# Performance work log

Measured on AMD Instinct MI355X. Metric: run time of the kernel, lower is better.

Reference implementation:

```python
import jax, jax.numpy as jnp
import numpy as np

B, S, P = 16, 1024, 1024
D, H, HD = 128, 8, 16      # embed_dim, num_heads, head_dim (qkv_dim)
MS = 32                    # ms_hidden_dim
E = 524288                 # number of edges
TANH_CLIP = 10.0
TEMP = 1.0
EPS = 1e-9


def setup_inputs() -> dict:
    key = jax.random.key(0)
    ks = jax.random.split(key, 12)
    inv = lambda n: 1.0 / np.sqrt(n)
    return {
        "x1": jax.random.normal(ks[0], (B, S, D), jnp.float32),
        "x2": jax.random.normal(ks[1], (B, P, D), jnp.float32),
        "b_idx": jax.random.randint(ks[2], (E,), 0, B, jnp.int32),
        "s_idx": jax.random.randint(ks[3], (E,), 0, S, jnp.int32),
        "p_idx": jax.random.randint(ks[4], (E,), 0, P, jnp.int32),
        "w": jax.random.uniform(ks[5], (E,), jnp.float32),
        "Wqv1": jax.random.normal(ks[6], (D, 2 * D), jnp.float32) * inv(D),
        "Wkv2": jax.random.normal(ks[7], (D, 2 * D), jnp.float32) * inv(D),
        "Wo1": jax.random.normal(ks[8], (D, D), jnp.float32) * inv(D),
        "Wo2": jax.random.normal(ks[9], (D, D), jnp.float32) * inv(D),
        "msW1": jax.random.normal(ks[10], (H, 2, MS), jnp.float32) * inv(2),
        "msb1": jnp.zeros((H, MS), jnp.float32),
        "msW2": jax.random.normal(ks[11], (H, MS, 1), jnp.float32) * inv(MS),
        "msb2": jnp.zeros((H, 1), jnp.float32),
    }


def _mixed_scores(logits, w, msW1, msb1, msW2, msb2):
    # logits: [E, H], w: [E] -> per-head 2->MS->1 MLP (MatNet MixedScoreFF)
    mixed = jnp.stack([logits, jnp.broadcast_to(w[:, None], logits.shape)], axis=-1)  # [E,H,2]
    hid = jax.nn.relu(jnp.einsum('ehi,him->ehm', mixed, msW1) + msb1)  # [E,H,MS]
    out = (jnp.einsum('ehm,hmo->eho', hid, msW2) + msb2)[..., 0]       # [E,H]
    return TANH_CLIP * jnp.tanh(out) / TEMP


def _group_softmax_combine(logits, values, gid, num_groups):
    # logits: [E,H], values: [E,H,HD]; exp -> segment-sum denom -> weighted scatter
    el = jnp.exp(logits)
    denom = jax.ops.segment_sum(el, gid, num_segments=num_groups)      # [G,H]
    attn = el / (denom[gid] + EPS)                                      # [E,H]
    return jax.ops.segment_sum(attn[:, :, None] * values, gid, num_segments=num_groups)  # [G,H,HD]


def reference(x1, x2, b_idx, s_idx, p_idx, w, Wqv1, Wkv2, Wo1, Wo2, msW1, msb1, msW2, msb2):
    qv1 = (x1 @ Wqv1).reshape(B, S, 2, H, HD)   # [B,S,2,H,HD]
    kv2 = (x2 @ Wkv2).reshape(B, P, 2, H, HD)
    row_flat = b_idx * S + s_idx                # [E]
    col_flat = b_idx * P + p_idx
    qv1_e = qv1.reshape(B * S, 2, H, HD)[row_flat]   # [E,2,H,HD]
    kv2_e = kv2.reshape(B * P, 2, H, HD)[col_flat]
    q, v1 = qv1_e[:, 0], qv1_e[:, 1]
    k, v2 = kv2_e[:, 0], kv2_e[:, 1]
    logits = jnp.einsum('ehd,ehd->eh', q, k) / np.sqrt(HD).astype(np.float32)
    logits = _mixed_scores(logits, w, msW1, msb1, msW2, msb2)
    row_heads = _group_softmax_combine(logits, v2, row_flat, B * S)  # [B*S,H,HD]
    col_heads = _group_softmax_combine(logits, v1, col_flat, B * P)  # [B*P,H,HD]
    h1 = row_heads.reshape(B, S, H * HD) @ Wo1
    h2 = col_heads.reshape(B, P, H * HD) @ Wo2
    return h1, h2
```

## Files before the change

kernel.cpp:

```cpp
#include <hip/hip_runtime.h>
#include <hip/hip_fp16.h>
#include <math.h>

#define BB   16
#define SS   1024
#define PP   1024
#define HH   8
#define MSS  32
#define EE   524288
#define NROW (BB*SS)
#define NCOL (BB*PP)
#define ESTRIDE 5
#define NRWB 512
#define NB   128
#define CHUNK 4096
#define GCAP 96

#define GLL(gp, lp) __builtin_amdgcn_global_load_lds( \
    (const __attribute__((address_space(1))) void*)(gp), \
    (__attribute__((address_space(3))) void*)(lp), 16, 0, 0)

__global__ __launch_bounds__(256, 2) void proj_kernel(
        const float* __restrict__ x1, const float* __restrict__ x2,
        const float* __restrict__ Wqv1, const float* __restrict__ Wkv2,
        float* __restrict__ qf, float* __restrict__ kf,
        __half* __restrict__ v1h, __half* __restrict__ v2h) {
    __shared__ float As[64 * 132];
    __shared__ float Bs[2][16 * 256];
    int t = threadIdx.x;
    int bid = blockIdx.x;
    int matrix = bid >> 8;
    int mb = bid & 255;
    const float* A  = matrix ? x2 : x1;
    const float* Bm = matrix ? Wkv2 : Wqv1;
    const float* Arow = A + (size_t)mb * 64 * 128;

    int tx = t & 31, ty = t >> 5;
#pragma unroll
    for (int li = 0; li < 8; li++) {
        int idx = li * 256 + t;
        int r = idx >> 5, p = idx & 31;
        *(float4*)&As[r * 132 + 4 * p] = *(const float4*)(Arow + r * 128 + 4 * p);
    }
#pragma unroll
    for (int li = 0; li < 4; li++) {
        int idx = li * 256 + t;
        GLL(Bm + 4 * idx, &Bs[0][4 * idx]);
    }

    float4 accL[8], accR[8];
#pragma unroll
    for (int i = 0; i < 8; i++) {
        accL[i] = make_float4(0.f, 0.f, 0.f, 0.f);
        accR[i] = make_float4(0.f, 0.f, 0.f, 0.f);
    }

    __syncthreads();

    for (int kc = 0; kc < 8; kc++) {
        if (kc < 7) {
            const float* src = Bm + (size_t)(kc + 1) * 16 * 256;
            float* dst = Bs[(kc + 1) & 1];
#pragma unroll
            for (int li = 0; li < 4; li++) {
                int idx = li * 256 + t;
                GLL(src + 4 * idx, dst + 4 * idx);
            }
        }
        const float* Bcur = Bs[kc & 1];
#pragma unroll
        for (int kq = 0; kq < 4; kq++) {
            float4 a4[8];
#pragma unroll
            for (int i = 0; i < 8; i++)
                a4[i] = *(const float4*)&As[(ty + 8 * i) * 132 + kc * 16 + kq * 4];
#pragma unroll
            for (int kk = 0; kk < 4; kk++) {
                float4 bL = *(const float4*)&Bcur[(kq * 4 + kk) * 256 + 4 * tx];
                float4 bR = *(const float4*)&Bcur[(kq * 4 + kk) * 256 + 128 + 4 * tx];
#pragma unroll
                for (int i = 0; i < 8; i++) {
                    float av = ((const float*)&a4[i])[kk];
                    accL[i].x = fmaf(av, bL.x, accL[i].x);
                    accL[i].y = fmaf(av, bL.y, accL[i].y);
                    accL[i].z = fmaf(av, bL.z, accL[i].z);
                    accL[i].w = fmaf(av, bL.w, accL[i].w);
                    accR[i].x = fmaf(av, bR.x, accR[i].x);
                    accR[i].y = fmaf(av, bR.y, accR[i].y);
                    accR[i].z = fmaf(av, bR.z, accR[i].z);
                    accR[i].w = fmaf(av, bR.w, accR[i].w);
                }
            }
        }
        __syncthreads();
    }

    float* Cq = matrix ? kf : qf;
    __half* Cv = matrix ? v2h : v1h;
#pragma unroll
    for (int i = 0; i < 8; i++) {
        int row = mb * 64 + ty + 8 * i;
        *(float4*)(Cq + (size_t)row * 128 + 4 * tx) = accL[i];
        __half2* p = (__half2*)(Cv + (size_t)row * 128 + 4 * tx);
        p[0] = __halves2half2(__float2half(accR[i].x), __float2half(accR[i].y));
        p[1] = __halves2half2(__float2half(accR[i].z), __float2half(accR[i].w));
    }
}

__global__ __launch_bounds__(256) void outp_kernel(
        const float* __restrict__ rh, const float* __restrict__ ch,
        const float* __restrict__ Wo1, const float* __restrict__ Wo2,
        float* __restrict__ out) {
    __shared__ float As[64 * 132];
    __shared__ float Bs[2][16 * 128];
    int t = threadIdx.x;
    int matrix = blockIdx.x >> 8;
    int mb = blockIdx.x & 255;
    const float* A  = matrix ? ch : rh;
    const float* Bm = matrix ? Wo2 : Wo1;
    float* C = out + (size_t)matrix * NROW * 128;
    const float* Arow = A + (size_t)mb * 64 * 128;

    int tx = t & 31, ty = t >> 5;
#pragma unroll
    for (int li = 0; li < 8; li++) {
        int idx = li * 256 + t;
        int r = idx >> 5, p = idx & 31;
        *(float4*)&As[r * 132 + 4 * p] = *(const float4*)(Arow + r * 128 + 4 * p);
    }
#pragma unroll
    for (int li = 0; li < 2; li++) {
        int idx = li * 256 + t;
        GLL(Bm + 4 * idx, &Bs[0][4 * idx]);
    }

    float4 acc4[8];
#pragma unroll
    for (int i = 0; i < 8; i++) acc4[i] = make_float4(0.f, 0.f, 0.f, 0.f);

    __syncthreads();

    for (int kc = 0; kc < 8; kc++) {
        if (kc < 7) {
            const float* src = Bm + (size_t)(kc + 1) * 16 * 128;
            float* dst = Bs[(kc + 1) & 1];
#pragma unroll
            for (int li = 0; li < 2; li++) {
                int idx = li * 256 + t;
                GLL(src + 4 * idx, dst + 4 * idx);
            }
        }
        const float* Bcur = Bs[kc & 1];
#pragma unroll
        for (int kq = 0; kq < 4; kq++) {
            float4 a4[8];
#pragma unroll
            for (int i = 0; i < 8; i++)
                a4[i] = *(const float4*)&As[(ty + 8 * i) * 132 + kc * 16 + kq * 4];
#pragma unroll
            for (int kk = 0; kk < 4; kk++) {
                float4 b4 = *(const float4*)&Bcur[(kq * 4 + kk) * 128 + 4 * tx];
#pragma unroll
                for (int i = 0; i < 8; i++) {
                    float av = ((const float*)&a4[i])[kk];
                    acc4[i].x = fmaf(av, b4.x, acc4[i].x);
                    acc4[i].y = fmaf(av, b4.y, acc4[i].y);
                    acc4[i].z = fmaf(av, b4.z, acc4[i].z);
                    acc4[i].w = fmaf(av, b4.w, acc4[i].w);
                }
            }
        }
        __syncthreads();
    }

#pragma unroll
    for (int i = 0; i < 8; i++) {
        int row = mb * 64 + ty + 8 * i;
        *(float4*)(C + (size_t)row * 128 + 4 * tx) = acc4[i];
    }
}

__global__ __launch_bounds__(1024) void hist_kernel(
        const int* __restrict__ b_idx, const int* __restrict__ s_idx,
        const int* __restrict__ p_idx, unsigned int* __restrict__ ph) {
    __shared__ unsigned int lh[16384];
    int t = threadIdx.x;
#pragma unroll
    for (int i = 0; i < 16; i++) lh[t + 1024 * i] = 0;
    __syncthreads();
    int base = blockIdx.x * CHUNK;
#pragma unroll
    for (int k = 0; k < 4; k++) {
        int e = base + k * 1024 + t;
        int b = b_idx[e];
        int rbin = (b << 10) + s_idx[e];
        int cbin = 16384 + (b << 10) + p_idx[e];
        atomicAdd(&lh[rbin >> 1], 1u << (16 * (rbin & 1)));
        atomicAdd(&lh[cbin >> 1], 1u << (16 * (cbin & 1)));
    }
    __syncthreads();
    unsigned int* dst = ph + (size_t)blockIdx.x * 16384;
#pragma unroll
    for (int i = 0; i < 16; i++) dst[t + 1024 * i] = lh[t + 1024 * i];
}

__global__ __launch_bounds__(128) void scan1_kernel(
        const unsigned int* __restrict__ ph, int* __restrict__ pbase,
        int* __restrict__ tot) {
    int bin = blockIdx.x * 128 + threadIdx.x;
    int word = bin >> 1;
    int sh = 16 * (bin & 1);
    int run = 0;
#pragma unroll 8
    for (int j = 0; j < NB; j++) {
        unsigned int v = ph[(size_t)j * 16384 + word];
        pbase[(size_t)j * 32768 + bin] = run;
        run += (v >> sh) & 0xffff;
    }
    tot[bin] = run;
}

__global__ __launch_bounds__(1024) void scan2_kernel(
        const int* __restrict__ tot, int* __restrict__ offs) {
    __shared__ int sdata[1024];
    int side = blockIdx.x;
    int t = threadIdx.x;
    const int* c = tot + side * 16384;
    int* o = offs + side * (16384 + 1);
    int base = t * 16;
    int loc[16];
    int run = 0;
#pragma unroll
    for (int i = 0; i < 16; i++) { loc[i] = run; run += c[base + i]; }
    sdata[t] = run;
    __syncthreads();
    for (int st = 1; st < 1024; st <<= 1) {
        int v = (t >= st) ? sdata[t - st] : 0;
        __syncthreads();
        sdata[t] += v;
        __syncthreads();
    }
    int excl = sdata[t] - run;
#pragma unroll
    for (int i = 0; i < 16; i++) o[base + i] = excl + loc[i];
    if (t == 1023) o[16384] = sdata[1023];
}

__global__ __launch_bounds__(1024) void pos_kernel(
        const int* __restrict__ b_idx, const int* __restrict__ s_idx,
        const int* __restrict__ p_idx, const float* __restrict__ w,
        const int* __restrict__ pbase, const int* __restrict__ offs,
        int4* __restrict__ ebuf) {
    __shared__ int cur[16384];
    int t = threadIdx.x;
    {
        const int* src = pbase + (size_t)blockIdx.x * 32768 + 16384;
        const int* oc = offs + (16384 + 1);
#pragma unroll
        for (int i = 0; i < 16; i++) {
            int idx = t + 1024 * i;
            cur[idx] = oc[idx] + src[idx];
        }
    }
    __syncthreads();
    int base = blockIdx.x * CHUNK;
    int rowr[4], colr[4], pcr[4];
    float wr[4];
#pragma unroll
    for (int k = 0; k < 4; k++) {
        int e = base + k * 1024 + t;
        int b = b_idx[e];
        rowr[k] = (b << 10) + s_idx[e];
        colr[k] = (b << 10) + p_idx[e];
        wr[k] = w[e];
        pcr[k] = atomicAdd(&cur[colr[k]], 1);
    }
    __syncthreads();
    {
        const int* src = pbase + (size_t)blockIdx.x * 32768;
#pragma unroll
        for (int i = 0; i < 16; i++) {
            int idx = t + 1024 * i;
            cur[idx] = offs[idx] + src[idx];
        }
    }
    __syncthreads();
#pragma unroll
    for (int k = 0; k < 4; k++) {
        int pr = atomicAdd(&cur[rowr[k]], 1);
        ebuf[pr] = make_int4(rowr[k], colr[k], __float_as_int(wr[k]), pcr[k]);
    }
}

__global__ __launch_bounds__(256) void edge_kernel(
        const float* __restrict__ qf, const float* __restrict__ kf,
        const int4* __restrict__ ebuf, const int* __restrict__ offs_row,
        const float* __restrict__ msW1, const float* __restrict__ msb1,
        const float* __restrict__ msW2, const float* __restrict__ msb2,
        float* __restrict__ entr, float* __restrict__ entc) {
    __shared__ float4 sPk[8 * 33];
    __shared__ float sB2[8];
    int t = threadIdx.x;
    {
        int h = t >> 5, m = t & 31;
        sPk[h * 33 + m] = make_float4(msW1[h * 64 + m], msW1[h * 64 + 32 + m],
                                      msb1[h * 32 + m], msW2[h * 32 + m]);
    }
    if (t < 8) sB2[t] = msb2[t];
    __syncthreads();

    int x = blockIdx.x & 7;
    int ridx = blockIdx.x >> 3;
    int wv = t >> 6;
    int lane = t & 63;
    int l = lane & 7;
    int g = lane >> 3;

    int rl = ridx * 4 + wv;
    int row = ((x + ((rl >> 10) << 3)) << 10) + (rl & 1023);
    int s = offs_row[row];
    int cnt = offs_row[row + 1] - s;

    int hh = 2 * (l & 3) + (l >> 2);
    const float4* wp = &sPk[hh * 33];
    float bias2 = sB2[hh];

    const float4* qp4 = (const float4*)(qf + (size_t)row * 128);
    float4 q0 = qp4[l], q1 = qp4[8 + l], q2 = qp4[16 + l], q3 = qp4[24 + l];

    for (int j0 = 0; j0 < cnt; j0 += 8) {
        int j = j0 + g;
        if (j < cnt) {
            int pos = s + j;
            int4 rec = ebuf[pos];
            int col = rec.y;
            float we = __int_as_float(rec.z);
            int pc = rec.w;

            const float4* kp4 = (const float4*)(kf + (size_t)col * 128);
            float p0, p1, p2, p3;
            {
                float4 k4 = kp4[l];
                p0 = fmaf(q0.x, k4.x, fmaf(q0.y, k4.y, fmaf(q0.z, k4.z, q0.w * k4.w)));
            }
            {
                float4 k4 = kp4[8 + l];
                p1 = fmaf(q1.x, k4.x, fmaf(q1.y, k4.y, fmaf(q1.z, k4.z, q1.w * k4.w)));
            }
            {
                float4 k4 = kp4[16 + l];
                p2 = fmaf(q2.x, k4.x, fmaf(q2.y, k4.y, fmaf(q2.z, k4.z, q2.w * k4.w)));
            }
            {
                float4 k4 = kp4[24 + l];
                p3 = fmaf(q3.x, k4.x, fmaf(q3.y, k4.y, fmaf(q3.z, k4.z, q3.w * k4.w)));
            }
            p0 += __shfl_xor(p0, 1); p0 += __shfl_xor(p0, 2);
            p1 += __shfl_xor(p1, 1); p1 += __shfl_xor(p1, 2);
            p2 += __shfl_xor(p2, 1); p2 += __shfl_xor(p2, 2);
            p3 += __shfl_xor(p3, 1); p3 += __shfl_xor(p3, 2);

            int js = l & 3;
            float dot = js == 0 ? p0 : (js == 1 ? p1 : (js == 2 ? p2 : p3));
            float logit = dot * 0.25f;

            float outv = bias2;
#pragma unroll 4
            for (int m = 0; m < MSS; m++) {
                float4 c = wp[m];
                float hid = fmaf(logit, c.x, fmaf(we, c.y, c.z));
                hid = fmaxf(hid, 0.f);
                outv = fmaf(hid, c.w, outv);
            }
            float u  = __expf(outv + outv);
            float th = 1.0f - 2.0f * __builtin_amdgcn_rcpf(u + 1.0f);
            float ev = __expf(10.0f * th);
            __half evh = __float2half(ev);

            float* er = entr + (size_t)pos * ESTRIDE;
            float* ec = entc + (size_t)pc * ESTRIDE;
            ((__half*)er)[2 + hh] = evh;
            ((__half*)ec)[2 + hh] = evh;
            if (l == 0) {
                er[0] = __int_as_float(col);
                ec[0] = __int_as_float(row);
            }
        }
    }
}

__global__ __launch_bounds__(128) void combine_kernel(
        const float* __restrict__ entr, const float* __restrict__ entc,
        const int* __restrict__ offs_row, const int* __restrict__ offs_col,
        const __half* __restrict__ v1h, const __half* __restrict__ v2h,
        float* __restrict__ row_heads, float* __restrict__ col_heads) {
    __shared__ float sE[GCAP * ESTRIDE];
    int x = blockIdx.x & 7;
    int r = blockIdx.x >> 3;
    int which = r >> 10;
    int sidx = r & 1023;
    int b = x + ((which & 1) << 3);
    int gl = (b << 10) + sidx;

    int t = threadIdx.x;
    int h = t >> 4;
    const float* ent; const __half* vals; const int* offs; float* outp;
    if (which < 2) { ent = entr; vals = v2h; offs = offs_row; outp = row_heads; }
    else           { ent = entc; vals = v1h; offs = offs_col; outp = col_heads; }
    int s = offs[gl], e_ = offs[gl + 1];
    int cnt = e_ - s;
    int cap = cnt < GCAP ? cnt : GCAP;

    const float* gsrc = ent + (size_t)s * ESTRIDE;
    for (int i = t; i < cap * ESTRIDE; i += 128) sE[i] = gsrc[i];
    __syncthreads();

    float acc = 0.f, den = 0.f;
#pragma unroll 8
    for (int i = 0; i < cap; i++) {
        const float* en = &sE[i * ESTRIDE];
        int other = __float_as_int(en[0]);
        float ev = __half2float(((const __half*)en)[2 + h]);
        float v = __half2float(vals[(size_t)other * 128 + t]);
        acc = fmaf(ev, v, acc);
        den += ev;
    }
    for (int i = cap; i < cnt; i++) {
        const float* en = gsrc + (size_t)i * ESTRIDE;
        int other = __float_as_int(en[0]);
        float ev = __half2float(((const __half*)en)[2 + h]);
        float v = __half2float(vals[(size_t)other * 128 + t]);
        acc = fmaf(ev, v, acc);
        den += ev;
    }
    outp[(size_t)gl * 128 + t] = acc / (den + 1e-9f);
}

extern "C" void kernel_launch(void* const* d_in, const int* in_sizes, int n_in,
                              void* d_out, int out_size, void* d_ws, size_t ws_size,
                              hipStream_t stream) {
    const float* x1   = (const float*)d_in[0];
    const float* x2   = (const float*)d_in[1];
    const int* b_idx  = (const int*)d_in[2];
    const int* s_idx  = (const int*)d_in[3];
    const int* p_idx  = (const int*)d_in[4];
    const float* w    = (const float*)d_in[5];
    const float* Wqv1 = (const float*)d_in[6];
    const float* Wkv2 = (const float*)d_in[7];
    const float* Wo1  = (const float*)d_in[8];
    const float* Wo2  = (const float*)d_in[9];
    const float* msW1 = (const float*)d_in[10];
    const float* msb1 = (const float*)d_in[11];
    const float* msW2 = (const float*)d_in[12];
    const float* msb2 = (const float*)d_in[13];
    float* out = (float*)d_out;

    float* qf = (float*)d_ws;
    float* kf = qf + (size_t)NROW * 128;
    __half* v1h = (__half*)(kf + (size_t)NCOL * 128);
    __half* v2h = v1h + (size_t)NROW * 128;
    float* entr = (float*)(v2h + (size_t)NCOL * 128);
    float* entc = entr + (size_t)EE * ESTRIDE;
    float* row_heads = entc + (size_t)EE * ESTRIDE;
    float* col_heads = row_heads + (size_t)NROW * 128;
    int4* ebuf = (int4*)(col_heads + (size_t)NCOL * 128);
    int* offs = (int*)(ebuf + EE);
    int* tot  = offs + 2 * (16384 + 1);
    unsigned int* ph = (unsigned int*)entc;
    int* pbase = (int*)row_heads;

    hist_kernel<<<NB, 1024, 0, stream>>>(b_idx, s_idx, p_idx, ph);
    scan1_kernel<<<256, 128, 0, stream>>>(ph, pbase, tot);
    scan2_kernel<<<2, 1024, 0, stream>>>(tot, offs);
    pos_kernel<<<NB, 1024, 0, stream>>>(b_idx, s_idx, p_idx, w, pbase, offs, ebuf);

    proj_kernel<<<512, 256, 0, stream>>>(x1, x2, Wqv1, Wkv2, qf, kf, v1h, v2h);

    edge_kernel<<<8 * NRWB, 256, 0, stream>>>(
        qf, kf, ebuf, offs, msW1, msb1, msW2, msb2, entr, entc);

    combine_kernel<<<2 * NROW, 128, 0, stream>>>(
        entr, entc, offs, offs + (16384 + 1), v1h, v2h, row_heads, col_heads);

    outp_kernel<<<512, 256, 0, stream>>>(row_heads, col_heads, Wo1, Wo2, out);
}
```

Before: 241.9 us.

## Split mixed-score MLP hidden units across lane groups with shuffle exchange

The 32-unit hidden layer of the per-head mixed-score MLP was computed serially by each lane, each step reading packed weights from shared memory. Now each of the 8 lane groups holds 4 hidden units' weights in registers. Logits and edge weights are exchanged among groups via shuffles, and partial sums are shuffled back and reduced. This cuts per-lane arithmetic and LDS reads from 32 to 4 units per edge, at the cost of about 24 shuffles. The loop becomes branch-free with clamped indices so all lanes take part in the shuffles.

Measured after the change: 242.3 us. About the same (+0.2%).

```diff
diff --git a/kernel.cpp b/kernel.cpp
--- a/kernel.cpp
+++ b/kernel.cpp
@@ -322,61 +322,84 @@
     int cnt = offs_row[row + 1] - s;
 
     int hh = 2 * (l & 3) + (l >> 2);
-    const float4* wp = &sPk[hh * 33];
     float bias2 = sB2[hh];
+    float4 c0 = sPk[hh * 33 + 4 * g + 0];
+    float4 c1 = sPk[hh * 33 + 4 * g + 1];
+    float4 c2 = sPk[hh * 33 + 4 * g + 2];
+    float4 c3 = sPk[hh * 33 + 4 * g + 3];
 
     const float4* qp4 = (const float4*)(qf + (size_t)row * 128);
     float4 q0 = qp4[l], q1 = qp4[8 + l], q2 = qp4[16 + l], q3 = qp4[24 + l];
 
     for (int j0 = 0; j0 < cnt; j0 += 8) {
         int j = j0 + g;
-        if (j < cnt) {
-            int pos = s + j;
-            int4 rec = ebuf[pos];
-            int col = rec.y;
-            float we = __int_as_float(rec.z);
-            int pc = rec.w;
-
-            const float4* kp4 = (const float4*)(kf + (size_t)col * 128);
-            float p0, p1, p2, p3;
-            {
-                float4 k4 = kp4[l];
-                p0 = fmaf(q0.x, k4.x, fmaf(q0.y, k4.y, fmaf(q0.z, k4.z, q0.w * k4.w)));
-            }
-            {
-                float4 k4 = kp4[8 + l];
-                p1 = fmaf(q1.x, k4.x, fmaf(q1.y, k4.y, fmaf(q1.z, k4.z, q1.w * k4.w)));
-            }
-            {
-                float4 k4 = kp4[16 + l];
-                p2 = fmaf(q2.x, k4.x, fmaf(q2.y, k4.y, fmaf(q2.z, k4.z, q2.w * k4.w)));
-            }
-            {
-                float4 k4 = kp4[24 + l];
-                p3 = fmaf(q3.x, k4.x, fmaf(q3.y, k4.y, fmaf(q3.z, k4.z, q3.w * k4.w)));
-            }
-            p0 += __shfl_xor(p0, 1); p0 += __shfl_xor(p0, 2);
-            p1 += __shfl_xor(p1, 1); p1 += __shfl_xor(p1, 2);
-            p2 += __shfl_xor(p2, 1); p2 += __shfl_xor(p2, 2);
-            p3 += __shfl_xor(p3, 1); p3 += __shfl_xor(p3, 2);
-
-            int js = l & 3;
-            float dot = js == 0 ? p0 : (js == 1 ? p1 : (js == 2 ? p2 : p3));
-            float logit = dot * 0.25f;
-
-            float outv = bias2;
-#pragma unroll 4
-            for (int m = 0; m < MSS; m++) {
-                float4 c = wp[m];
-                float hid = fmaf(logit, c.x, fmaf(we, c.y, c.z));
-                hid = fmaxf(hid, 0.f);
-                outv = fmaf(hid, c.w, outv);
-            }
-            float u  = __expf(outv + outv);
-            float th = 1.0f - 2.0f * __builtin_amdgcn_rcpf(u + 1.0f);
-            float ev = __expf(10.0f * th);
-            __half evh = __float2half(ev);
-
+        bool valid = j < cnt;
+        int jc = valid ? j : (cnt - 1);
+        int pos = s + jc;
+        int4 rec = ebuf[pos];
+        int col = rec.y;
+        float we = __int_as_float(rec.z);
+        int pc = rec.w;
+
+        const float4* kp4 = (const float4*)(kf + (size_t)col * 128);
+        float p0, p1, p2, p3;
+        {
+            float4 k4 = kp4[l];
+            p0 = fmaf(q0.x, k4.x, fmaf(q0.y, k4.y, fmaf(q0.z, k4.z, q0.w * k4.w)));
+        }
+        {
+            float4 k4 = kp4[8 + l];
+            p1 = fmaf(q1.x, k4.x, fmaf(q1.y, k4.y, fmaf(q1.z, k4.z, q1.w * k4.w)));
+        }
+        {
+            float4 k4 = kp4[16 + l];
+            p2 = fmaf(q2.x, k4.x, fmaf(q2.y, k4.y, fmaf(q2.z, k4.z, q2.w * k4.w)));
+        }
+        {
+            float4 k4 = kp4[24 + l];
+            p3 = fmaf(q3.x, k4.x, fmaf(q3.y, k4.y, fmaf(q3.z, k4.z, q3.w * k4.w)));
+        }
+        p0 += __shfl_xor(p0, 1); p0 += __shfl_xor(p0, 2);
+        p1 += __shfl_xor(p1, 1); p1 += __shfl_xor(p1, 2);
+        p2 += __shfl_xor(p2, 1); p2 += __shfl_xor(p2, 2);
+        p3 += __shfl_xor(p3, 1); p3 += __shfl_xor(p3, 2);
+
+        int js = l & 3;
+        float dot = js == 0 ? p0 : (js == 1 ? p1 : (js == 2 ? p2 : p3));
+        float lg = valid ? dot * 0.25f : 0.f;
+        float wez = valid ? we : 0.f;
+
+        float pr[8];
+#pragma unroll
+        for (int r = 0; r < 8; r++) {
+            int src = (((g + r) & 7) << 3) + l;
+            float lgr = __shfl(lg, src);
+            float wer = __shfl(wez, src);
+            float acc = 0.f;
+            float hid;
+            hid = fmaf(lgr, c0.x, fmaf(wer, c0.y, c0.z));
+            acc = fmaf(fmaxf(hid, 0.f), c0.w, acc);
+            hid = fmaf(lgr, c1.x, fmaf(wer, c1.y, c1.z));
+            acc = fmaf(fmaxf(hid, 0.f), c1.w, acc);
+            hid = fmaf(lgr, c2.x, fmaf(wer, c2.y, c2.z));
+            acc = fmaf(fmaxf(hid, 0.f), c2.w, acc);
+            hid = fmaf(lgr, c3.x, fmaf(wer, c3.y, c3.z));
+            acc = fmaf(fmaxf(hid, 0.f), c3.w, acc);
+            pr[r] = acc;
+        }
+        float outv = bias2;
+#pragma unroll
+        for (int r = 0; r < 8; r++) {
+            int src = (((g - r) & 7) << 3) + l;
+            outv += __shfl(pr[r], src);
+        }
+
+        float u  = __expf(outv + outv);
+        float th = 1.0f - 2.0f * __builtin_amdgcn_rcpf(u + 1.0f);
+        float ev = __expf(10.0f * th);
+        __half evh = __float2half(ev);
+
+        if (valid) {
             float* er = entr + (size_t)pos * ESTRIDE;
             float* ec = entc + (size_t)pc * ESTRIDE;
             ((__half*)er)[2 + hh] = evh;
```
